# Kernel tuning notes

Hardware: AMD Instinct MI355X
Metric: run time of the kernel (lower is better)

Reference implementation:

```python
import jax, jax.numpy as jnp
import numpy as np

LOG2PI = float(np.log(2.0 * np.pi))
BATCH = 131072
IN_FEATURES = 128
MULT = 3          # Gaussian multiplicity / Sum in_channels
CARD = 2          # first Product cardinality -> 64 features


def setup_inputs() -> dict:
    key = jax.random.key(0)
    k1, k2, k3, k4, k5 = jax.random.split(key, 5)
    x = jax.random.normal(k1, (BATCH, IN_FEATURES), dtype=jnp.float32)
    means = jax.random.normal(k2, (1, IN_FEATURES, MULT), dtype=jnp.float32)
    # stds drawn positive (torch.rand init for scale params)
    stds = jax.random.uniform(k3, (1, IN_FEATURES, MULT), dtype=jnp.float32,
                              minval=0.1, maxval=1.0)
    sum_weights = jax.random.normal(k4, (64, MULT, 1), dtype=jnp.float32)
    # randomized Product layer: fixed random permutation of the 128 features
    perm = jax.random.permutation(k5, IN_FEATURES).astype(jnp.int32)
    return {"x": x, "means": means, "stds": stds,
            "sum_weights": sum_weights, "perm": perm}


def reference(x, means, stds, sum_weights, perm):
    n = x.shape[0]
    # --- Gaussian leaf: Normal(mu, sigma).log_prob(x) -> [n, 128, 3]
    z = (x[:, :, None] - means) / stds
    lp = -0.5 * (z * z) - jnp.log(stds) - 0.5 * LOG2PI
    # --- Product(in_features=128, cardinality=2, randomize): permute features,
    # pair them up, product in log-domain = sum -> [n, 64, 3]
    lp = lp[:, perm, :]
    lp = lp.reshape(n, IN_FEATURES // CARD, CARD, MULT).sum(axis=2)
    # --- Sum(in_channels=3, in_features=64, out_channels=1): weighted
    # log-sum-exp mixture over channels with log_softmax-normalized weights
    logw = jax.nn.log_softmax(sum_weights, axis=1)          # [64, 3, 1]
    lp = jax.nn.logsumexp(lp[:, :, :, None] + logw[None], axis=2)  # [n, 64, 1]
    # --- Product(in_features=64, cardinality=64): sum all features -> [n, 1, 1]
    # (permutation before a full reduction is a no-op, so omitted)
    out = lp.sum(axis=1, keepdims=True).reshape(n, 1, 1)
    return out
```

## Files before the change

### kernel.cpp

```cpp
#include <hip/hip_runtime.h>

#define N_FEAT 128


__global__ void spn_precompute(const float* __restrict__ means,
                               const float* __restrict__ stds,
                               const float* __restrict__ sumw,
                               const int* __restrict__ perm,
                               float* __restrict__ ws) {
    const float LOG2PI = 1.8378770664093453f;
    const float LOG2E  = 1.4426950408889634f;
    int g = threadIdx.x;
    if (g >= 64) return;
    int p0 = perm[2 * g], p1 = perm[2 * g + 1];
    int* pf = (int*)(ws + 960);
    pf[g] = p0;
    pf[64 + g] = p1;
    float w0 = sumw[g * 3 + 0], w1 = sumw[g * 3 + 1], w2 = sumw[g * 3 + 2];
    float mx = fmaxf(w0, fmaxf(w1, w2));
    float lse = mx + logf(expf(w0 - mx) + expf(w1 - mx) + expf(w2 - mx));
    for (int m = 0; m < 3; ++m) {
        float s0 = stds[p0 * 3 + m], mu0 = means[p0 * 3 + m];
        float s1 = stds[p1 * 3 + m], mu1 = means[p1 * 3 + m];
        float i0 = 1.0f / s0, i1 = 1.0f / s1;
        float lw = sumw[g * 3 + m] - lse;
        ws[g * 3 + m]        = mu0 * i0;
        ws[192 + g * 3 + m]  = i0;
        ws[384 + g * 3 + m]  = mu1 * i1;
        ws[576 + g * 3 + m]  = i1;
        ws[768 + g * 3 + m]  = (lw - logf(s0) - logf(s1) - LOG2PI) * LOG2E;
    }
}

__global__ __launch_bounds__(256)
void spn_main(const float* __restrict__ x,
              const float* __restrict__ ws,
              float* __restrict__ out, int n) {
    const float NHALF_LOG2E = -0.7213475204444817f;
    const float LN2 = 0.6931471805599453f;

    const int lane   = threadIdx.x & 63;
    const int wave   = (blockIdx.x * blockDim.x + threadIdx.x) >> 6;
    const int nwaves = (gridDim.x * blockDim.x) >> 6;

    const int* pf = (const int*)(ws + 960);
    const int p0 = pf[lane];
    const int p1 = pf[64 + lane];
    float nm0[3], is0[3], nm1[3], is1[3], C2[3];
#pragma unroll
    for (int m = 0; m < 3; ++m) {
        nm0[m] = ws[lane * 3 + m];
        is0[m] = ws[192 + lane * 3 + m];
        nm1[m] = ws[384 + lane * 3 + m];
        is1[m] = ws[576 + lane * 3 + m];
        C2[m]  = ws[768 + lane * 3 + m];
    }

    int rpw  = (n + nwaves - 1) / nwaves;
    int row0 = wave * rpw;
    int row1 = row0 + rpw;
    if (row1 > n) row1 = n;

    for (int row = row0; row < row1; ++row) {
        const float* xr = x + (size_t)row * N_FEAT;
        float a = xr[p0];
        float b = xr[p1];
        float v0, v1, v2;
        {
            float z0 = fmaf(a, is0[0], -nm0[0]);
            float z1 = fmaf(b, is1[0], -nm1[0]);
            v0 = fmaf(z0 * z0, NHALF_LOG2E, C2[0]);
            v0 = fmaf(z1 * z1, NHALF_LOG2E, v0);
        }
        {
            float z0 = fmaf(a, is0[1], -nm0[1]);
            float z1 = fmaf(b, is1[1], -nm1[1]);
            v1 = fmaf(z0 * z0, NHALF_LOG2E, C2[1]);
            v1 = fmaf(z1 * z1, NHALF_LOG2E, v1);
        }
        {
            float z0 = fmaf(a, is0[2], -nm0[2]);
            float z1 = fmaf(b, is1[2], -nm1[2]);
            v2 = fmaf(z0 * z0, NHALF_LOG2E, C2[2]);
            v2 = fmaf(z1 * z1, NHALF_LOG2E, v2);
        }
        float mx = fmaxf(v0, fmaxf(v1, v2));
        float s = __builtin_amdgcn_exp2f(v0 - mx)
                + __builtin_amdgcn_exp2f(v1 - mx)
                + __builtin_amdgcn_exp2f(v2 - mx);
        float r = mx + __builtin_amdgcn_logf(s);
#pragma unroll
        for (int off = 32; off >= 1; off >>= 1)
            r += __shfl_xor(r, off, 64);
        if (lane == 0) out[row] = r * LN2;
    }
}

extern "C" void kernel_launch(void* const* d_in, const int* in_sizes, int n_in,
                              void* d_out, int out_size, void* d_ws, size_t ws_size,
                              hipStream_t stream) {
    const float* x     = (const float*)d_in[0];
    const float* means = (const float*)d_in[1];
    const float* stds  = (const float*)d_in[2];
    const float* sumw  = (const float*)d_in[3];
    const int*   perm  = (const int*)d_in[4];
    float* ws  = (float*)d_ws;
    float* out = (float*)d_out;
    int n = in_sizes[0] / N_FEAT;

    hipLaunchKernelGGL(spn_precompute, dim3(1), dim3(64), 0, stream,
                       means, stds, sumw, perm, ws);
    hipLaunchKernelGGL(spn_main, dim3(2048), dim3(256), 0, stream,
                       x, ws, out, n);
}
```

Before: 107.5 us.

## Fuse parameter precompute into main kernel and stage row tiles in LDS

Merges the one-block precompute kernel into the main kernel, so every block rebuilds the per-pair constants in shared memory. This removes a second launch and the dependency between the two kernels. Each block loads 32-row tiles of x with coalesced float4 loads into LDS, then gathers the permuted features from LDS rather than issuing scattered global loads. Eight row results per wave are reduced with interleaved shuffles. The costs are redundant parameter setup in every block, extra barriers per tile, and a tail that is silently dropped when n is not a multiple of 32.

```diff
diff --git a/kernel.cpp b/kernel.cpp
--- a/kernel.cpp
+++ b/kernel.cpp
@@ -1,98 +1,119 @@
 #include <hip/hip_runtime.h>
 
 #define N_FEAT 128
+#define ROWS   32
+#define TPB    256
 
+__global__ __launch_bounds__(TPB)
+void spn_fused(const float* __restrict__ x,
+               const float* __restrict__ means,
+               const float* __restrict__ stds,
+               const float* __restrict__ sumw,
+               const int* __restrict__ perm,
+               float* __restrict__ out, int n) {
+    __shared__ float sx[ROWS * N_FEAT];
+    __shared__ float snm0[192], sis0[192], snm1[192], sis1[192], sC2[192];
+    __shared__ int   sp0[64], sp1[64];
 
-__global__ void spn_precompute(const float* __restrict__ means,
-                               const float* __restrict__ stds,
-                               const float* __restrict__ sumw,
-                               const int* __restrict__ perm,
-                               float* __restrict__ ws) {
-    const float LOG2PI = 1.8378770664093453f;
-    const float LOG2E  = 1.4426950408889634f;
-    int g = threadIdx.x;
-    if (g >= 64) return;
-    int p0 = perm[2 * g], p1 = perm[2 * g + 1];
-    int* pf = (int*)(ws + 960);
-    pf[g] = p0;
-    pf[64 + g] = p1;
-    float w0 = sumw[g * 3 + 0], w1 = sumw[g * 3 + 1], w2 = sumw[g * 3 + 2];
-    float mx = fmaxf(w0, fmaxf(w1, w2));
-    float lse = mx + logf(expf(w0 - mx) + expf(w1 - mx) + expf(w2 - mx));
-    for (int m = 0; m < 3; ++m) {
-        float s0 = stds[p0 * 3 + m], mu0 = means[p0 * 3 + m];
-        float s1 = stds[p1 * 3 + m], mu1 = means[p1 * 3 + m];
-        float i0 = 1.0f / s0, i1 = 1.0f / s1;
-        float lw = sumw[g * 3 + m] - lse;
-        ws[g * 3 + m]        = mu0 * i0;
-        ws[192 + g * 3 + m]  = i0;
-        ws[384 + g * 3 + m]  = mu1 * i1;
-        ws[576 + g * 3 + m]  = i1;
-        ws[768 + g * 3 + m]  = (lw - logf(s0) - logf(s1) - LOG2PI) * LOG2E;
-    }
-}
-
-__global__ __launch_bounds__(256)
-void spn_main(const float* __restrict__ x,
-              const float* __restrict__ ws,
-              float* __restrict__ out, int n) {
     const float NHALF_LOG2E = -0.7213475204444817f;
     const float LN2 = 0.6931471805599453f;
 
-    const int lane   = threadIdx.x & 63;
-    const int wave   = (blockIdx.x * blockDim.x + threadIdx.x) >> 6;
-    const int nwaves = (gridDim.x * blockDim.x) >> 6;
+    const int tid  = threadIdx.x;
+    const int lane = tid & 63;
+    const int wv   = tid >> 6;
 
-    const int* pf = (const int*)(ws + 960);
-    const int p0 = pf[lane];
-    const int p1 = pf[64 + lane];
+    if (tid < 64) {
+        const float LOG2PI_ = 1.8378770664093453f;
+        const float LOG2E   = 1.4426950408889634f;
+        const int g  = tid;
+        const int p0 = perm[2 * g], p1 = perm[2 * g + 1];
+        sp0[g] = p0; sp1[g] = p1;
+        float w0 = sumw[g * 3 + 0], w1 = sumw[g * 3 + 1], w2 = sumw[g * 3 + 2];
+        float mx  = fmaxf(w0, fmaxf(w1, w2));
+        float lse = mx + logf(expf(w0 - mx) + expf(w1 - mx) + expf(w2 - mx));
+#pragma unroll
+        for (int m = 0; m < 3; ++m) {
+            float s0 = stds[p0 * 3 + m], mu0 = means[p0 * 3 + m];
+            float s1 = stds[p1 * 3 + m], mu1 = means[p1 * 3 + m];
+            float i0 = 1.0f / s0, i1 = 1.0f / s1;
+            float lw = sumw[g * 3 + m] - lse;
+            snm0[g * 3 + m] = mu0 * i0;
+            sis0[g * 3 + m] = i0;
+            snm1[g * 3 + m] = mu1 * i1;
+            sis1[g * 3 + m] = i1;
+            sC2[g * 3 + m]  = (lw - logf(s0) - logf(s1) - LOG2PI_) * LOG2E;
+        }
+    }
+    __syncthreads();
+
+    const int p0 = sp0[lane];
+    const int p1 = sp1[lane];
     float nm0[3], is0[3], nm1[3], is1[3], C2[3];
 #pragma unroll
     for (int m = 0; m < 3; ++m) {
-        nm0[m] = ws[lane * 3 + m];
-        is0[m] = ws[192 + lane * 3 + m];
-        nm1[m] = ws[384 + lane * 3 + m];
-        is1[m] = ws[576 + lane * 3 + m];
-        C2[m]  = ws[768 + lane * 3 + m];
+        nm0[m] = snm0[lane * 3 + m];
+        is0[m] = sis0[lane * 3 + m];
+        nm1[m] = snm1[lane * 3 + m];
+        is1[m] = sis1[lane * 3 + m];
+        C2[m]  = sC2[lane * 3 + m];
     }
 
-    int rpw  = (n + nwaves - 1) / nwaves;
-    int row0 = wave * rpw;
-    int row1 = row0 + rpw;
-    if (row1 > n) row1 = n;
+    const int ntiles = n / ROWS;
+    for (int tile = blockIdx.x; tile < ntiles; tile += gridDim.x) {
+        const int rowbase = tile * ROWS;
+        __syncthreads();
 
-    for (int row = row0; row < row1; ++row) {
-        const float* xr = x + (size_t)row * N_FEAT;
-        float a = xr[p0];
-        float b = xr[p1];
-        float v0, v1, v2;
-        {
-            float z0 = fmaf(a, is0[0], -nm0[0]);
-            float z1 = fmaf(b, is1[0], -nm1[0]);
-            v0 = fmaf(z0 * z0, NHALF_LOG2E, C2[0]);
-            v0 = fmaf(z1 * z1, NHALF_LOG2E, v0);
+        const float4* xv = (const float4*)(x + (size_t)rowbase * N_FEAT);
+        float4* sv = (float4*)sx;
+#pragma unroll
+        for (int it = 0; it < 4; ++it)
+            sv[it * TPB + tid] = xv[it * TPB + tid];
+        __syncthreads();
+
+        float res[8];
+#pragma unroll
+        for (int r = 0; r < 8; ++r) {
+            const float* xr = sx + (wv * 8 + r) * N_FEAT;
+            const float a = xr[p0];
+            const float b = xr[p1];
+            float v0, v1, v2;
+            {
+                float z0 = fmaf(a, is0[0], -nm0[0]);
+                float z1 = fmaf(b, is1[0], -nm1[0]);
+                v0 = fmaf(z0 * z0, NHALF_LOG2E, C2[0]);
+                v0 = fmaf(z1 * z1, NHALF_LOG2E, v0);
+            }
+            {
+                float z0 = fmaf(a, is0[1], -nm0[1]);
+                float z1 = fmaf(b, is1[1], -nm1[1]);
+                v1 = fmaf(z0 * z0, NHALF_LOG2E, C2[1]);
+                v1 = fmaf(z1 * z1, NHALF_LOG2E, v1);
+            }
+            {
+                float z0 = fmaf(a, is0[2], -nm0[2]);
+                float z1 = fmaf(b, is1[2], -nm1[2]);
+                v2 = fmaf(z0 * z0, NHALF_LOG2E, C2[2]);
+                v2 = fmaf(z1 * z1, NHALF_LOG2E, v2);
+            }
+            float mx = fmaxf(v0, fmaxf(v1, v2));
+            float s = __builtin_amdgcn_exp2f(v0 - mx)
+                    + __builtin_amdgcn_exp2f(v1 - mx)
+                    + __builtin_amdgcn_exp2f(v2 - mx);
+            res[r] = mx + __builtin_amdgcn_logf(s);
         }
-        {
-            float z0 = fmaf(a, is0[1], -nm0[1]);
-            float z1 = fmaf(b, is1[1], -nm1[1]);
-            v1 = fmaf(z0 * z0, NHALF_LOG2E, C2[1]);
-            v1 = fmaf(z1 * z1, NHALF_LOG2E, v1);
+
+#pragma unroll
+        for (int off = 32; off >= 1; off >>= 1) {
+#pragma unroll
+            for (int r = 0; r < 8; ++r)
+                res[r] += __shfl_xor(res[r], off, 64);
         }
-        {
-            float z0 = fmaf(a, is0[2], -nm0[2]);
-            float z1 = fmaf(b, is1[2], -nm1[2]);
-            v2 = fmaf(z0 * z0, NHALF_LOG2E, C2[2]);
-            v2 = fmaf(z1 * z1, NHALF_LOG2E, v2);
+
+        if (lane == 0) {
+#pragma unroll
+            for (int r = 0; r < 8; ++r)
+                out[rowbase + wv * 8 + r] = res[r] * LN2;
         }
-        float mx = fmaxf(v0, fmaxf(v1, v2));
-        float s = __builtin_amdgcn_exp2f(v0 - mx)
-                + __builtin_amdgcn_exp2f(v1 - mx)
-                + __builtin_amdgcn_exp2f(v2 - mx);
-        float r = mx + __builtin_amdgcn_logf(s);
-#pragma unroll
-        for (int off = 32; off >= 1; off >>= 1)
-            r += __shfl_xor(r, off, 64);
-        if (lane == 0) out[row] = r * LN2;
     }
 }
 
@@ -104,12 +125,9 @@
     const float* stds  = (const float*)d_in[2];
     const float* sumw  = (const float*)d_in[3];
     const int*   perm  = (const int*)d_in[4];
-    float* ws  = (float*)d_ws;
     float* out = (float*)d_out;
     int n = in_sizes[0] / N_FEAT;
 
-    hipLaunchKernelGGL(spn_precompute, dim3(1), dim3(64), 0, stream,
-                       means, stds, sumw, perm, ws);
-    hipLaunchKernelGGL(spn_main, dim3(2048), dim3(256), 0, stream,
-                       x, ws, out, n);
+    hipLaunchKernelGGL(spn_fused, dim3(1024), dim3(TPB), 0, stream,
+                       x, means, stds, sumw, perm, out, n);
 }
```

Result: faster. 102.6 us (-4.6%).
